# Performance work log

Measured on AMD Instinct MI355X. Metric: run time of the kernel, lower is better.

Reference implementation:

```python
import jax, jax.numpy as jnp
import numpy as np

N_NODES = 50000
TEMPERATURE = 1.0


def _gcn_norm(edge_index, n_nodes):
    src, dst = edge_index[0], edge_index[1]
    ones = jnp.ones(src.shape[0], dtype=jnp.float32)
    deg = 1.0 + jax.ops.segment_sum(ones, dst, num_segments=n_nodes)  # +1 for self loop
    dinv = jax.lax.rsqrt(deg)
    norm_e = dinv[src] * dinv[dst]          # symmetric edge norm
    self_norm = 1.0 / deg                   # self-loop contribution deg^-1
    return norm_e, self_norm


def _gcn_layer(x, W, b, src, dst, norm_e, self_norm, n_nodes):
    h = x @ W                                # [N, d_out]
    msg = h[src] * norm_e[:, None]           # gather + scale, [E, d_out]
    agg = jax.ops.segment_sum(msg, dst, num_segments=n_nodes)
    return agg + h * self_norm[:, None] + b


def setup_inputs() -> dict:
    key = jax.random.key(0)
    ks = jax.random.split(key, 8)
    n_feat, n_hid, n_layer, n_class = 128, 64, 4, 40
    n_edges = 800000
    x = jax.random.normal(ks[0], (N_NODES, n_feat), dtype=jnp.float32)
    edge_index = jax.random.randint(ks[1], (2, n_edges), 0, N_NODES, dtype=jnp.int64)
    s0 = 1.0 / np.sqrt(n_feat)
    s1 = 1.0 / np.sqrt(n_hid)
    W0 = jax.random.normal(ks[2], (n_feat, n_hid), dtype=jnp.float32) * s0
    b0 = jnp.zeros((n_hid,), dtype=jnp.float32)
    Ws = jax.random.normal(ks[3], (n_layer - 1, n_hid, n_hid), dtype=jnp.float32) * s1
    bs = jnp.zeros((n_layer - 1, n_hid), dtype=jnp.float32)
    Wout = jax.random.normal(ks[4], (n_hid, n_class), dtype=jnp.float32) * s1
    bout = jnp.zeros((n_class,), dtype=jnp.float32)
    return {"x": x, "W0": W0, "b0": b0, "Ws": Ws, "bs": bs,
            "Wout": Wout, "bout": bout, "edge_index": edge_index}


def reference(x, W0, b0, Ws, bs, Wout, bout, edge_index):
    src, dst = edge_index[0], edge_index[1]
    norm_e, self_norm = _gcn_norm(edge_index, N_NODES)

    x_ = jax.lax.stop_gradient(x)  # x.clone().detach()
    hs, hs_ = [], []
    n_layer = Ws.shape[0] + 1
    for l in range(n_layer):
        W = W0 if l == 0 else Ws[l - 1]
        b = b0 if l == 0 else bs[l - 1]
        h = _gcn_layer(x, W, b, src, dst, norm_e, self_norm, N_NODES)
        h_ = _gcn_layer(x_, W, b, src, dst, norm_e, self_norm, N_NODES)
        # vanilla skip: x <- h; ReLU; dropout disabled (eval mode)
        x = jax.nn.relu(h)
        x_ = jax.nn.relu(h_)
        hs.append(x)
        hs_.append(x_)

    H = jnp.stack(hs, axis=1)    # [N, L, d]
    H_ = jnp.stack(hs_, axis=1)  # [N, L, d]
    # local dot-product kernel attention over layers
    scores = jnp.sum(H * H_, axis=-1) / TEMPERATURE          # [N, L]
    alpha = jax.nn.softmax(scores, axis=-1)                   # [N, L]
    h = jnp.einsum("nl,nld->nd", alpha, H)                    # [N, d]
    return h @ Wout + bout                                     # [N, n_class]
```

## Files before the change

kernel.cpp:

```cpp
#include <hip/hip_runtime.h>
#include <hip/hip_fp16.h>

#define N_NODES 50000
#define N_HID   64
#define N_LAYER 4
#define N_CLASS 40
#define N_EDGES 800000

#define BSHIFT 8
#define BSIZE  256
#define NBUCK  ((N_NODES + BSIZE - 1) / BSIZE)
#define BPAD   16
#define EPT    16
#define BKCHUNK (256 * EPT)
#define NBBLK  ((N_EDGES + BKCHUNK - 1) / BKCHUNK)

#define SCAP  5120
#define PBK   (SCAP + 15 * BSIZE)
#define DUMMY N_NODES


__global__ void k_zerob(int* __restrict__ bcur, __half* __restrict__ hdA,
                        __half* __restrict__ hdB) {
    int t = threadIdx.x;
    if (t < NBUCK) bcur[t * BPAD] = t * SCAP;
    if (t < 64) {
        hdA[(size_t)N_NODES * 64 + t] = __float2half(0.f);
        hdB[(size_t)N_NODES * 64 + t] = __float2half(0.f);
    }
}


__global__ void k_bucket(const int* __restrict__ src, const int* __restrict__ dst,
                         int* __restrict__ bcur, unsigned int* __restrict__ stag) {
    __shared__ int lhist[NBUCK];
    __shared__ int gbase[NBUCK];
    int t = threadIdx.x;
    for (int i = t; i < NBUCK; i += 256) lhist[i] = 0;
    __syncthreads();

    int base = blockIdx.x * BKCHUNK;
    unsigned int rec[EPT];
    int br[EPT];
#pragma unroll
    for (int i = 0; i < EPT; i++) {
        int e = base + i * 256 + t;
        if (e < N_EDGES) {
            int d = dst[e], s = src[e];
            int b = d >> BSHIFT;
            int r = atomicAdd(&lhist[b], 1);
            rec[i] = ((unsigned int)d << 16) | (unsigned int)s;
            br[i]  = (b << 16) | r;
        } else {
            br[i] = -1;
        }
    }
    __syncthreads();
    for (int i = t; i < NBUCK; i += 256) {
        int c = lhist[i];
        gbase[i] = c ? atomicAdd(&bcur[i * BPAD], c) : 0;
    }
    __syncthreads();
#pragma unroll
    for (int i = 0; i < EPT; i++) {
        if (br[i] >= 0) {
            int b = br[i] >> 16, r = br[i] & 0xffff;
            stag[gbase[b] + r] = rec[i];
        }
    }
}


__global__ void k_csr2(const unsigned int* __restrict__ stag, const int* __restrict__ bcur,
                       int* __restrict__ cnt, int* __restrict__ pcurg,
                       float* __restrict__ dinv, unsigned short* __restrict__ csr16) {
    __shared__ int lcnt[BSIZE], ltmp[BSIZE], lcur[BSIZE];
    int b = blockIdx.x, t = threadIdx.x;
    int bstart = b * SCAP;
    int bend   = bcur[b * BPAD];
    lcnt[t] = 0;
    __syncthreads();
    for (int i = bstart + t; i < bend; i += 256)
        atomicAdd(&lcnt[(stag[i] >> 16) & (BSIZE - 1)], 1);
    __syncthreads();
    int v = lcnt[t];
    int p = (v + 15) & ~15;
    ltmp[t] = p;
    __syncthreads();
    for (int off = 1; off < 256; off <<= 1) {
        int u = (t >= off) ? ltmp[t - off] : 0;
        __syncthreads();
        ltmp[t] += u;
        __syncthreads();
    }
    int pstart = b * PBK + ltmp[t] - p;
    lcur[t] = pstart;
    int node = (b << BSHIFT) + t;
    if (node < N_NODES) {
        cnt[node]   = v;
        pcurg[node] = pstart;
        dinv[node]  = rsqrtf((float)(v + 1));
    }
    __syncthreads();
    for (int i = bstart + t; i < bend; i += 256) {
        unsigned int rec = stag[i];
        int pos = atomicAdd(&lcur[(rec >> 16) & (BSIZE - 1)], 1);
        csr16[pos] = (unsigned short)rec;
    }
    for (int i = v; i < p; i++)
        csr16[pstart + i] = (unsigned short)DUMMY;
}


__global__ __launch_bounds__(256) void k_gemm0(const float* __restrict__ A,
                                               const float* __restrict__ W,
                                               const float* __restrict__ dinv,
                                               __half* __restrict__ hd) {
    __shared__ float As[16][128];
    int tid = threadIdx.x;
    int j  = tid & 63;
    int nl = tid >> 6;
    int node0 = blockIdx.x * 16;

    const float4* srcp = (const float4*)(A + (size_t)node0 * 128);
    float4* dstp = (float4*)&As[0][0];
    for (int idx = tid; idx < 16 * 128 / 4; idx += 256) dstp[idx] = srcp[idx];
    __syncthreads();

    float acc[4] = {0.f, 0.f, 0.f, 0.f};
#pragma unroll
    for (int k = 0; k < 128; k += 4) {
        float4 a0 = *(const float4*)&As[nl * 4 + 0][k];
        float4 a1 = *(const float4*)&As[nl * 4 + 1][k];
        float4 a2 = *(const float4*)&As[nl * 4 + 2][k];
        float4 a3 = *(const float4*)&As[nl * 4 + 3][k];
        float w0 = W[(k + 0) * 64 + j];
        float w1 = W[(k + 1) * 64 + j];
        float w2 = W[(k + 2) * 64 + j];
        float w3 = W[(k + 3) * 64 + j];
        acc[0] = fmaf(a0.w, w3, fmaf(a0.z, w2, fmaf(a0.y, w1, fmaf(a0.x, w0, acc[0]))));
        acc[1] = fmaf(a1.w, w3, fmaf(a1.z, w2, fmaf(a1.y, w1, fmaf(a1.x, w0, acc[1]))));
        acc[2] = fmaf(a2.w, w3, fmaf(a2.z, w2, fmaf(a2.y, w1, fmaf(a2.x, w0, acc[2]))));
        acc[3] = fmaf(a3.w, w3, fmaf(a3.z, w2, fmaf(a3.y, w1, fmaf(a3.x, w0, acc[3]))));
    }
#pragma unroll
    for (int i = 0; i < 4; i++) {
        int n = node0 + nl * 4 + i;
        hd[(size_t)n * 64 + j] = __float2half(acc[i] * dinv[n]);
    }
}


__device__ __forceinline__ float4 agg_node16(const uint2* __restrict__ hd2,
                                             const int* __restrict__ cnt,
                                             const int* __restrict__ pcur,
                                             const unsigned short* __restrict__ csr16,
                                             int n, int f, int par) {
    int k = pcur[n] + par * 4;
    int iters = (cnt[n] + 15) >> 4;
    float s0 = 0.f, s1 = 0.f, s2 = 0.f, s3 = 0.f;
    for (int it = 0; it < iters; ++it, k += 16) {
        uint2 idx = *(const uint2*)(csr16 + k);
        int a0 = idx.x & 0xffff, a1 = idx.x >> 16;
        int a2 = idx.y & 0xffff, a3 = idx.y >> 16;
        uint2 r0 = hd2[(size_t)a0 * 16 + f];
        uint2 r1 = hd2[(size_t)a1 * 16 + f];
        uint2 r2 = hd2[(size_t)a2 * 16 + f];
        uint2 r3 = hd2[(size_t)a3 * 16 + f];
        float2 p0 = __half22float2(*(const __half2*)&r0.x), q0 = __half22float2(*(const __half2*)&r0.y);
        float2 p1 = __half22float2(*(const __half2*)&r1.x), q1 = __half22float2(*(const __half2*)&r1.y);
        float2 p2 = __half22float2(*(const __half2*)&r2.x), q2 = __half22float2(*(const __half2*)&r2.y);
        float2 p3 = __half22float2(*(const __half2*)&r3.x), q3 = __half22float2(*(const __half2*)&r3.y);
        s0 += (p0.x + p1.x) + (p2.x + p3.x);
        s1 += (p0.y + p1.y) + (p2.y + p3.y);
        s2 += (q0.x + q1.x) + (q2.x + q3.x);
        s3 += (q0.y + q1.y) + (q2.y + q3.y);
    }
    s0 += __shfl_xor(s0, 16, 64); s1 += __shfl_xor(s1, 16, 64);
    s2 += __shfl_xor(s2, 16, 64); s3 += __shfl_xor(s3, 16, 64);
    s0 += __shfl_xor(s0, 32, 64); s1 += __shfl_xor(s1, 32, 64);
    s2 += __shfl_xor(s2, 32, 64); s3 += __shfl_xor(s3, 32, 64);
    return make_float4(s0, s1, s2, s3);
}


__global__ __launch_bounds__(256) void k_fused(const uint2* __restrict__ hd2_in,
                                               const float* __restrict__ b,
                                               const float* __restrict__ dinv,
                                               const int* __restrict__ cnt,
                                               const int* __restrict__ pcur,
                                               const unsigned short* __restrict__ csr16,
                                               const float* __restrict__ W,
                                               __half* __restrict__ hs_out,
                                               __half* __restrict__ hd_out) {
    __shared__ float As[4][64];
    int tid = threadIdx.x;
    int w = tid >> 6, lane = tid & 63;
    int f = lane & 15, par = lane >> 4;
    int node0 = blockIdx.x * 4;
    int n = node0 + w;

    float4 s = agg_node16(hd2_in, cnt, pcur, csr16, n, f, par);
    if (par == 0) {
        float dv = dinv[n];
        uint2 sr = hd2_in[(size_t)n * 16 + f];
        float2 sp = __half22float2(*(const __half2*)&sr.x);
        float2 sq = __half22float2(*(const __half2*)&sr.y);
        float o0 = fmaxf(fmaf(s.x + sp.x, dv, b[f * 4 + 0]), 0.f);
        float o1 = fmaxf(fmaf(s.y + sp.y, dv, b[f * 4 + 1]), 0.f);
        float o2 = fmaxf(fmaf(s.z + sq.x, dv, b[f * 4 + 2]), 0.f);
        float o3 = fmaxf(fmaf(s.w + sq.y, dv, b[f * 4 + 3]), 0.f);
        *(float4*)&As[w][f * 4] = make_float4(o0, o1, o2, o3);
        __half2 h0 = __halves2half2(__float2half(o0), __float2half(o1));
        __half2 h1 = __halves2half2(__float2half(o2), __float2half(o3));
        uint2 pk;
        pk.x = *(const unsigned int*)&h0;
        pk.y = *(const unsigned int*)&h1;
        ((uint2*)hs_out)[(size_t)n * 16 + f] = pk;
    }
    __syncthreads();

    if (tid < 64) {
        float acc[4] = {0.f, 0.f, 0.f, 0.f};
#pragma unroll
        for (int k = 0; k < 64; k += 4) {
            float4 a0 = *(const float4*)&As[0][k];
            float4 a1 = *(const float4*)&As[1][k];
            float4 a2 = *(const float4*)&As[2][k];
            float4 a3 = *(const float4*)&As[3][k];
            float w0 = W[(k + 0) * 64 + tid];
            float w1 = W[(k + 1) * 64 + tid];
            float w2 = W[(k + 2) * 64 + tid];
            float w3 = W[(k + 3) * 64 + tid];
            acc[0] = fmaf(a0.w, w3, fmaf(a0.z, w2, fmaf(a0.y, w1, fmaf(a0.x, w0, acc[0]))));
            acc[1] = fmaf(a1.w, w3, fmaf(a1.z, w2, fmaf(a1.y, w1, fmaf(a1.x, w0, acc[1]))));
            acc[2] = fmaf(a2.w, w3, fmaf(a2.z, w2, fmaf(a2.y, w1, fmaf(a2.x, w0, acc[2]))));
            acc[3] = fmaf(a3.w, w3, fmaf(a3.z, w2, fmaf(a3.y, w1, fmaf(a3.x, w0, acc[3]))));
        }
#pragma unroll
        for (int i = 0; i < 4; i++) {
            int nn = node0 + i;
            hd_out[(size_t)nn * 64 + tid] = __float2half(acc[i] * dinv[nn]);
        }
    }
}


__global__ __launch_bounds__(256) void k_last(const uint2* __restrict__ hd2_in,
                                              const float* __restrict__ b,
                                              const float* __restrict__ dinv,
                                              const int* __restrict__ cnt,
                                              const int* __restrict__ pcur,
                                              const unsigned short* __restrict__ csr16,
                                              const __half* __restrict__ hs16,
                                              const float* __restrict__ Wout,
                                              const float* __restrict__ bout,
                                              float* __restrict__ out) {
    __shared__ float As[4][64];
    int tid = threadIdx.x;
    int w = tid >> 6, lane = tid & 63;
    int f = lane & 15, par = lane >> 4;
    int node0 = blockIdx.x * 4;
    int n = node0 + w;

    float4 s = agg_node16(hd2_in, cnt, pcur, csr16, n, f, par);
    if (par == 0) {
        float dv = dinv[n];
        uint2 sr = hd2_in[(size_t)n * 16 + f];
        float2 sp = __half22float2(*(const __half2*)&sr.x);
        float2 sq = __half22float2(*(const __half2*)&sr.y);
        float o0 = fmaxf(fmaf(s.x + sp.x, dv, b[f * 4 + 0]), 0.f);
        float o1 = fmaxf(fmaf(s.y + sp.y, dv, b[f * 4 + 1]), 0.f);
        float o2 = fmaxf(fmaf(s.z + sq.x, dv, b[f * 4 + 2]), 0.f);
        float o3 = fmaxf(fmaf(s.w + sq.y, dv, b[f * 4 + 3]), 0.f);
        *(float4*)&As[w][f * 4] = make_float4(o0, o1, o2, o3);
    }
    __builtin_amdgcn_wave_barrier();

    float v[N_LAYER], sc[N_LAYER];
#pragma unroll
    for (int l = 0; l < 3; l++) {
        float val = __half2float(hs16[((size_t)l * N_NODES + n) * 64 + lane]);
        v[l]  = val;
        sc[l] = val * val;
    }
    v[3]  = As[w][lane];
    sc[3] = v[3] * v[3];
#pragma unroll
    for (int off = 32; off > 0; off >>= 1) {
#pragma unroll
        for (int l = 0; l < N_LAYER; l++) sc[l] += __shfl_xor(sc[l], off, 64);
    }
    float m = fmaxf(fmaxf(sc[0], sc[1]), fmaxf(sc[2], sc[3]));
    float e[N_LAYER];
    float sum = 0.f;
#pragma unroll
    for (int l = 0; l < N_LAYER; l++) { e[l] = __expf(sc[l] - m); sum += e[l]; }
    float inv = 1.f / sum;
    float bl = 0.f;
#pragma unroll
    for (int l = 0; l < N_LAYER; l++) bl = fmaf(e[l] * inv, v[l], bl);
    As[w][lane] = bl;
    __syncthreads();

    if (tid < 64 && tid < N_CLASS) {
        float acc[4] = {bout[tid], bout[tid], bout[tid], bout[tid]};
#pragma unroll
        for (int k = 0; k < 64; k += 4) {
            float4 a0 = *(const float4*)&As[0][k];
            float4 a1 = *(const float4*)&As[1][k];
            float4 a2 = *(const float4*)&As[2][k];
            float4 a3 = *(const float4*)&As[3][k];
            float w0 = Wout[(k + 0) * N_CLASS + tid];
            float w1 = Wout[(k + 1) * N_CLASS + tid];
            float w2 = Wout[(k + 2) * N_CLASS + tid];
            float w3 = Wout[(k + 3) * N_CLASS + tid];
            acc[0] = fmaf(a0.w, w3, fmaf(a0.z, w2, fmaf(a0.y, w1, fmaf(a0.x, w0, acc[0]))));
            acc[1] = fmaf(a1.w, w3, fmaf(a1.z, w2, fmaf(a1.y, w1, fmaf(a1.x, w0, acc[1]))));
            acc[2] = fmaf(a2.w, w3, fmaf(a2.z, w2, fmaf(a2.y, w1, fmaf(a2.x, w0, acc[2]))));
            acc[3] = fmaf(a3.w, w3, fmaf(a3.z, w2, fmaf(a3.y, w1, fmaf(a3.x, w0, acc[3]))));
        }
#pragma unroll
        for (int i = 0; i < 4; i++)
            out[(size_t)(node0 + i) * N_CLASS + tid] = acc[i];
    }
}


extern "C" void kernel_launch(void* const* d_in, const int* in_sizes, int n_in,
                              void* d_out, int out_size, void* d_ws, size_t ws_size,
                              hipStream_t stream) {
    const float* x    = (const float*)d_in[0];
    const float* W0   = (const float*)d_in[1];
    const float* b0   = (const float*)d_in[2];
    const float* Ws   = (const float*)d_in[3];
    const float* bs   = (const float*)d_in[4];
    const float* Wout = (const float*)d_in[5];
    const float* bout = (const float*)d_in[6];
    const int*   ei   = (const int*)d_in[7];
    const int* src = ei;
    const int* dst = ei + N_EDGES;
    float* out = (float*)d_out;

    int*            cnt   = (int*)d_ws;
    int*            pcur  = cnt + N_NODES;
    int*            bcur  = pcur + N_NODES;
    float*          dinv  = (float*)(bcur + NBUCK * BPAD);
    unsigned short* csr16 = (unsigned short*)(dinv + N_NODES);
    __half*         hdA   = (__half*)(csr16 + (size_t)NBUCK * PBK);
    __half*         hdB   = hdA + (size_t)(N_NODES + 1) * 64;
    __half*         hs16  = hdB + (size_t)(N_NODES + 1) * 64;
    unsigned int*   stag  = (unsigned int*)hs16;

    k_zerob <<<1, 256, 0, stream>>>(bcur, hdA, hdB);
    k_bucket<<<NBBLK, 256, 0, stream>>>(src, dst, bcur, stag);
    k_csr2  <<<NBUCK, 256, 0, stream>>>(stag, bcur, cnt, pcur, dinv, csr16);

    k_gemm0<<<N_NODES / 16, 256, 0, stream>>>(x, W0, dinv, hdA);

    const int NB = N_NODES / 4;

    k_fused<<<NB, 256, 0, stream>>>((const uint2*)hdA, b0, dinv, cnt, pcur, csr16,
                                    Ws + 0 * 64 * 64, hs16 + (size_t)0 * N_NODES * 64, hdB);
    k_fused<<<NB, 256, 0, stream>>>((const uint2*)hdB, bs + 0 * 64, dinv, cnt, pcur, csr16,
                                    Ws + 1 * 64 * 64, hs16 + (size_t)1 * N_NODES * 64, hdA);
    k_fused<<<NB, 256, 0, stream>>>((const uint2*)hdA, bs + 1 * 64, dinv, cnt, pcur, csr16,
                                    Ws + 2 * 64 * 64, hs16 + (size_t)2 * N_NODES * 64, hdB);
    k_last <<<NB, 256, 0, stream>>>((const uint2*)hdB, bs + 2 * 64, dinv, cnt, pcur, csr16,
                                    hs16, Wout, bout, out);
}
```

Baseline: 188.2 us.

## Split feature table into half-width column slabs and unfuse aggregation from GEMM

Stores the per-layer scaled features as two 32-column fp16 slabs, so each gather pass reads a smaller table (about 3.2 MB) that can stay in cache during the random neighbour gathers. Aggregation becomes its own kernel, run twice per layer (once per slab). The dense 64x64 transform moves to a separate GEMM kernel, and attention plus the output projection move to a standalone kernel. In exchange the CSR index stream is read twice per layer, there are more kernel launches, and hs is written and read back through global memory between the stages.

```diff
diff --git a/kernel.cpp b/kernel.cpp
--- a/kernel.cpp
+++ b/kernel.cpp
@@ -20,13 +20,13 @@
 #define DUMMY N_NODES
 
 
-__global__ void k_zerob(int* __restrict__ bcur, __half* __restrict__ hdA,
-                        __half* __restrict__ hdB) {
+__global__ void k_zerob(int* __restrict__ bcur, __half* __restrict__ hdLo,
+                        __half* __restrict__ hdHi) {
     int t = threadIdx.x;
     if (t < NBUCK) bcur[t * BPAD] = t * SCAP;
-    if (t < 64) {
-        hdA[(size_t)N_NODES * 64 + t] = __float2half(0.f);
-        hdB[(size_t)N_NODES * 64 + t] = __float2half(0.f);
+    if (t < 32) {
+        hdLo[(size_t)N_NODES * 32 + t] = __float2half(0.f);
+        hdHi[(size_t)N_NODES * 32 + t] = __float2half(0.f);
     }
 }
 
@@ -115,7 +115,8 @@
 __global__ __launch_bounds__(256) void k_gemm0(const float* __restrict__ A,
                                                const float* __restrict__ W,
                                                const float* __restrict__ dinv,
-                                               __half* __restrict__ hd) {
+                                               __half* __restrict__ hdLo,
+                                               __half* __restrict__ hdHi) {
     __shared__ float As[16][128];
     int tid = threadIdx.x;
     int j  = tid & 63;
@@ -146,146 +147,126 @@
 #pragma unroll
     for (int i = 0; i < 4; i++) {
         int n = node0 + nl * 4 + i;
-        hd[(size_t)n * 64 + j] = __float2half(acc[i] * dinv[n]);
-    }
-}
-
-
-__device__ __forceinline__ float4 agg_node16(const uint2* __restrict__ hd2,
+        float v = acc[i] * dinv[n];
+        if (j < 32) hdLo[(size_t)n * 32 + j]      = __float2half(v);
+        else        hdHi[(size_t)n * 32 + j - 32] = __float2half(v);
+    }
+}
+
+
+__global__ __launch_bounds__(256) void k_agg(const uint2* __restrict__ tbl,
+                                             const float* __restrict__ b32,
+                                             const float* __restrict__ dinv,
                                              const int* __restrict__ cnt,
                                              const int* __restrict__ pcur,
                                              const unsigned short* __restrict__ csr16,
-                                             int n, int f, int par) {
-    int k = pcur[n] + par * 4;
+                                             uint2* __restrict__ hs_out) {
+    int tid = threadIdx.x;
+    int w = tid >> 6, lane = tid & 63;
+    int f = lane & 7;
+    int par = lane >> 3;
+    int n = blockIdx.x * 4 + w;
+
+    int k = pcur[n] + par * 2;
     int iters = (cnt[n] + 15) >> 4;
     float s0 = 0.f, s1 = 0.f, s2 = 0.f, s3 = 0.f;
     for (int it = 0; it < iters; ++it, k += 16) {
-        uint2 idx = *(const uint2*)(csr16 + k);
-        int a0 = idx.x & 0xffff, a1 = idx.x >> 16;
-        int a2 = idx.y & 0xffff, a3 = idx.y >> 16;
-        uint2 r0 = hd2[(size_t)a0 * 16 + f];
-        uint2 r1 = hd2[(size_t)a1 * 16 + f];
-        uint2 r2 = hd2[(size_t)a2 * 16 + f];
-        uint2 r3 = hd2[(size_t)a3 * 16 + f];
+        unsigned int idx = *(const unsigned int*)(csr16 + k);
+        int a0 = idx & 0xffff, a1 = idx >> 16;
+        uint2 r0 = tbl[(size_t)a0 * 8 + f];
+        uint2 r1 = tbl[(size_t)a1 * 8 + f];
         float2 p0 = __half22float2(*(const __half2*)&r0.x), q0 = __half22float2(*(const __half2*)&r0.y);
         float2 p1 = __half22float2(*(const __half2*)&r1.x), q1 = __half22float2(*(const __half2*)&r1.y);
-        float2 p2 = __half22float2(*(const __half2*)&r2.x), q2 = __half22float2(*(const __half2*)&r2.y);
-        float2 p3 = __half22float2(*(const __half2*)&r3.x), q3 = __half22float2(*(const __half2*)&r3.y);
-        s0 += (p0.x + p1.x) + (p2.x + p3.x);
-        s1 += (p0.y + p1.y) + (p2.y + p3.y);
-        s2 += (q0.x + q1.x) + (q2.x + q3.x);
-        s3 += (q0.y + q1.y) + (q2.y + q3.y);
-    }
+        s0 += p0.x + p1.x;
+        s1 += p0.y + p1.y;
+        s2 += q0.x + q1.x;
+        s3 += q0.y + q1.y;
+    }
+    s0 += __shfl_xor(s0, 8, 64);  s1 += __shfl_xor(s1, 8, 64);
+    s2 += __shfl_xor(s2, 8, 64);  s3 += __shfl_xor(s3, 8, 64);
     s0 += __shfl_xor(s0, 16, 64); s1 += __shfl_xor(s1, 16, 64);
     s2 += __shfl_xor(s2, 16, 64); s3 += __shfl_xor(s3, 16, 64);
     s0 += __shfl_xor(s0, 32, 64); s1 += __shfl_xor(s1, 32, 64);
     s2 += __shfl_xor(s2, 32, 64); s3 += __shfl_xor(s3, 32, 64);
-    return make_float4(s0, s1, s2, s3);
-}
-
-
-__global__ __launch_bounds__(256) void k_fused(const uint2* __restrict__ hd2_in,
-                                               const float* __restrict__ b,
-                                               const float* __restrict__ dinv,
-                                               const int* __restrict__ cnt,
-                                               const int* __restrict__ pcur,
-                                               const unsigned short* __restrict__ csr16,
-                                               const float* __restrict__ W,
-                                               __half* __restrict__ hs_out,
-                                               __half* __restrict__ hd_out) {
-    __shared__ float As[4][64];
-    int tid = threadIdx.x;
-    int w = tid >> 6, lane = tid & 63;
-    int f = lane & 15, par = lane >> 4;
-    int node0 = blockIdx.x * 4;
-    int n = node0 + w;
-
-    float4 s = agg_node16(hd2_in, cnt, pcur, csr16, n, f, par);
+
     if (par == 0) {
         float dv = dinv[n];
-        uint2 sr = hd2_in[(size_t)n * 16 + f];
+        uint2 sr = tbl[(size_t)n * 8 + f];
         float2 sp = __half22float2(*(const __half2*)&sr.x);
         float2 sq = __half22float2(*(const __half2*)&sr.y);
-        float o0 = fmaxf(fmaf(s.x + sp.x, dv, b[f * 4 + 0]), 0.f);
-        float o1 = fmaxf(fmaf(s.y + sp.y, dv, b[f * 4 + 1]), 0.f);
-        float o2 = fmaxf(fmaf(s.z + sq.x, dv, b[f * 4 + 2]), 0.f);
-        float o3 = fmaxf(fmaf(s.w + sq.y, dv, b[f * 4 + 3]), 0.f);
-        *(float4*)&As[w][f * 4] = make_float4(o0, o1, o2, o3);
+        float o0 = fmaxf(fmaf(s0 + sp.x, dv, b32[f * 4 + 0]), 0.f);
+        float o1 = fmaxf(fmaf(s1 + sp.y, dv, b32[f * 4 + 1]), 0.f);
+        float o2 = fmaxf(fmaf(s2 + sq.x, dv, b32[f * 4 + 2]), 0.f);
+        float o3 = fmaxf(fmaf(s3 + sq.y, dv, b32[f * 4 + 3]), 0.f);
         __half2 h0 = __halves2half2(__float2half(o0), __float2half(o1));
         __half2 h1 = __halves2half2(__float2half(o2), __float2half(o3));
         uint2 pk;
         pk.x = *(const unsigned int*)&h0;
         pk.y = *(const unsigned int*)&h1;
-        ((uint2*)hs_out)[(size_t)n * 16 + f] = pk;
-    }
-    __syncthreads();
-
-    if (tid < 64) {
-        float acc[4] = {0.f, 0.f, 0.f, 0.f};
-#pragma unroll
-        for (int k = 0; k < 64; k += 4) {
-            float4 a0 = *(const float4*)&As[0][k];
-            float4 a1 = *(const float4*)&As[1][k];
-            float4 a2 = *(const float4*)&As[2][k];
-            float4 a3 = *(const float4*)&As[3][k];
-            float w0 = W[(k + 0) * 64 + tid];
-            float w1 = W[(k + 1) * 64 + tid];
-            float w2 = W[(k + 2) * 64 + tid];
-            float w3 = W[(k + 3) * 64 + tid];
-            acc[0] = fmaf(a0.w, w3, fmaf(a0.z, w2, fmaf(a0.y, w1, fmaf(a0.x, w0, acc[0]))));
-            acc[1] = fmaf(a1.w, w3, fmaf(a1.z, w2, fmaf(a1.y, w1, fmaf(a1.x, w0, acc[1]))));
-            acc[2] = fmaf(a2.w, w3, fmaf(a2.z, w2, fmaf(a2.y, w1, fmaf(a2.x, w0, acc[2]))));
-            acc[3] = fmaf(a3.w, w3, fmaf(a3.z, w2, fmaf(a3.y, w1, fmaf(a3.x, w0, acc[3]))));
-        }
-#pragma unroll
-        for (int i = 0; i < 4; i++) {
-            int nn = node0 + i;
-            hd_out[(size_t)nn * 64 + tid] = __float2half(acc[i] * dinv[nn]);
-        }
-    }
-}
-
-
-__global__ __launch_bounds__(256) void k_last(const uint2* __restrict__ hd2_in,
-                                              const float* __restrict__ b,
+        hs_out[(size_t)n * 16 + f] = pk;
+    }
+}
+
+
+__global__ __launch_bounds__(256) void k_gemm(const uint2* __restrict__ hs,
+                                              const float* __restrict__ W,
                                               const float* __restrict__ dinv,
-                                              const int* __restrict__ cnt,
-                                              const int* __restrict__ pcur,
-                                              const unsigned short* __restrict__ csr16,
-                                              const __half* __restrict__ hs16,
+                                              __half* __restrict__ hdLo,
+                                              __half* __restrict__ hdHi) {
+    __shared__ float As[16][64];
+    int tid = threadIdx.x;
+    int node0 = blockIdx.x * 16;
+
+    uint2 h = hs[(size_t)node0 * 16 + tid];
+    float2 pa = __half22float2(*(const __half2*)&h.x);
+    float2 pb = __half22float2(*(const __half2*)&h.y);
+    *(float4*)&As[tid >> 4][(tid & 15) * 4] = make_float4(pa.x, pa.y, pb.x, pb.y);
+    __syncthreads();
+
+    int j  = tid & 63;
+    int nl = tid >> 6;
+    float acc[4] = {0.f, 0.f, 0.f, 0.f};
+#pragma unroll
+    for (int k = 0; k < 64; k += 4) {
+        float4 a0 = *(const float4*)&As[nl * 4 + 0][k];
+        float4 a1 = *(const float4*)&As[nl * 4 + 1][k];
+        float4 a2 = *(const float4*)&As[nl * 4 + 2][k];
+        float4 a3 = *(const float4*)&As[nl * 4 + 3][k];
+        float w0 = W[(k + 0) * 64 + j];
+        float w1 = W[(k + 1) * 64 + j];
+        float w2 = W[(k + 2) * 64 + j];
+        float w3 = W[(k + 3) * 64 + j];
+        acc[0] = fmaf(a0.w, w3, fmaf(a0.z, w2, fmaf(a0.y, w1, fmaf(a0.x, w0, acc[0]))));
+        acc[1] = fmaf(a1.w, w3, fmaf(a1.z, w2, fmaf(a1.y, w1, fmaf(a1.x, w0, acc[1]))));
+        acc[2] = fmaf(a2.w, w3, fmaf(a2.z, w2, fmaf(a2.y, w1, fmaf(a2.x, w0, acc[2]))));
+        acc[3] = fmaf(a3.w, w3, fmaf(a3.z, w2, fmaf(a3.y, w1, fmaf(a3.x, w0, acc[3]))));
+    }
+#pragma unroll
+    for (int i = 0; i < 4; i++) {
+        int n = node0 + nl * 4 + i;
+        float v = acc[i] * dinv[n];
+        if (j < 32) hdLo[(size_t)n * 32 + j]      = __float2half(v);
+        else        hdHi[(size_t)n * 32 + j - 32] = __float2half(v);
+    }
+}
+
+
+__global__ __launch_bounds__(256) void k_attn(const __half* __restrict__ hs16,
                                               const float* __restrict__ Wout,
                                               const float* __restrict__ bout,
                                               float* __restrict__ out) {
-    __shared__ float As[4][64];
-    int tid = threadIdx.x;
-    int w = tid >> 6, lane = tid & 63;
-    int f = lane & 15, par = lane >> 4;
-    int node0 = blockIdx.x * 4;
-    int n = node0 + w;
-
-    float4 s = agg_node16(hd2_in, cnt, pcur, csr16, n, f, par);
-    if (par == 0) {
-        float dv = dinv[n];
-        uint2 sr = hd2_in[(size_t)n * 16 + f];
-        float2 sp = __half22float2(*(const __half2*)&sr.x);
-        float2 sq = __half22float2(*(const __half2*)&sr.y);
-        float o0 = fmaxf(fmaf(s.x + sp.x, dv, b[f * 4 + 0]), 0.f);
-        float o1 = fmaxf(fmaf(s.y + sp.y, dv, b[f * 4 + 1]), 0.f);
-        float o2 = fmaxf(fmaf(s.z + sq.x, dv, b[f * 4 + 2]), 0.f);
-        float o3 = fmaxf(fmaf(s.w + sq.y, dv, b[f * 4 + 3]), 0.f);
-        *(float4*)&As[w][f * 4] = make_float4(o0, o1, o2, o3);
-    }
-    __builtin_amdgcn_wave_barrier();
+    __shared__ float blend[4][64];
+    int j  = threadIdx.x & 63;
+    int nl = threadIdx.x >> 6;
+    int n  = blockIdx.x * 4 + nl;
 
     float v[N_LAYER], sc[N_LAYER];
 #pragma unroll
-    for (int l = 0; l < 3; l++) {
-        float val = __half2float(hs16[((size_t)l * N_NODES + n) * 64 + lane]);
+    for (int l = 0; l < N_LAYER; l++) {
+        float val = __half2float(hs16[((size_t)l * N_NODES + n) * 64 + j]);
         v[l]  = val;
         sc[l] = val * val;
     }
-    v[3]  = As[w][lane];
-    sc[3] = v[3] * v[3];
 #pragma unroll
     for (int off = 32; off > 0; off >>= 1) {
 #pragma unroll
@@ -300,29 +281,15 @@
     float bl = 0.f;
 #pragma unroll
     for (int l = 0; l < N_LAYER; l++) bl = fmaf(e[l] * inv, v[l], bl);
-    As[w][lane] = bl;
-    __syncthreads();
-
-    if (tid < 64 && tid < N_CLASS) {
-        float acc[4] = {bout[tid], bout[tid], bout[tid], bout[tid]};
-#pragma unroll
-        for (int k = 0; k < 64; k += 4) {
-            float4 a0 = *(const float4*)&As[0][k];
-            float4 a1 = *(const float4*)&As[1][k];
-            float4 a2 = *(const float4*)&As[2][k];
-            float4 a3 = *(const float4*)&As[3][k];
-            float w0 = Wout[(k + 0) * N_CLASS + tid];
-            float w1 = Wout[(k + 1) * N_CLASS + tid];
-            float w2 = Wout[(k + 2) * N_CLASS + tid];
-            float w3 = Wout[(k + 3) * N_CLASS + tid];
-            acc[0] = fmaf(a0.w, w3, fmaf(a0.z, w2, fmaf(a0.y, w1, fmaf(a0.x, w0, acc[0]))));
-            acc[1] = fmaf(a1.w, w3, fmaf(a1.z, w2, fmaf(a1.y, w1, fmaf(a1.x, w0, acc[1]))));
-            acc[2] = fmaf(a2.w, w3, fmaf(a2.z, w2, fmaf(a2.y, w1, fmaf(a2.x, w0, acc[2]))));
-            acc[3] = fmaf(a3.w, w3, fmaf(a3.z, w2, fmaf(a3.y, w1, fmaf(a3.x, w0, acc[3]))));
-        }
-#pragma unroll
-        for (int i = 0; i < 4; i++)
-            out[(size_t)(node0 + i) * N_CLASS + tid] = acc[i];
+    blend[nl][j] = bl;
+    __syncthreads();
+
+    if (j < N_CLASS) {
+        float o = bout[j];
+#pragma unroll
+        for (int k = 0; k < 64; k++)
+            o = fmaf(blend[nl][k], Wout[k * N_CLASS + j], o);
+        out[(size_t)n * N_CLASS + j] = o;
     }
 }
 
@@ -347,25 +314,31 @@
     int*            bcur  = pcur + N_NODES;
     float*          dinv  = (float*)(bcur + NBUCK * BPAD);
     unsigned short* csr16 = (unsigned short*)(dinv + N_NODES);
-    __half*         hdA   = (__half*)(csr16 + (size_t)NBUCK * PBK);
-    __half*         hdB   = hdA + (size_t)(N_NODES + 1) * 64;
-    __half*         hs16  = hdB + (size_t)(N_NODES + 1) * 64;
+    __half*         hdLo  = (__half*)(csr16 + (size_t)NBUCK * PBK);
+    __half*         hdHi  = hdLo + (size_t)(N_NODES + 1) * 32;
+    __half*         hs16  = hdHi + (size_t)(N_NODES + 1) * 32;
     unsigned int*   stag  = (unsigned int*)hs16;
 
-    k_zerob <<<1, 256, 0, stream>>>(bcur, hdA, hdB);
+    k_zerob <<<1, 256, 0, stream>>>(bcur, hdLo, hdHi);
     k_bucket<<<NBBLK, 256, 0, stream>>>(src, dst, bcur, stag);
     k_csr2  <<<NBUCK, 256, 0, stream>>>(stag, bcur, cnt, pcur, dinv, csr16);
 
-    k_gemm0<<<N_NODES / 16, 256, 0, stream>>>(x, W0, dinv, hdA);
+    k_gemm0<<<N_NODES / 16, 256, 0, stream>>>(x, W0, dinv, hdLo, hdHi);
 
     const int NB = N_NODES / 4;
 
-    k_fused<<<NB, 256, 0, stream>>>((const uint2*)hdA, b0, dinv, cnt, pcur, csr16,
-                                    Ws + 0 * 64 * 64, hs16 + (size_t)0 * N_NODES * 64, hdB);
-    k_fused<<<NB, 256, 0, stream>>>((const uint2*)hdB, bs + 0 * 64, dinv, cnt, pcur, csr16,
-                                    Ws + 1 * 64 * 64, hs16 + (size_t)1 * N_NODES * 64, hdA);
-    k_fused<<<NB, 256, 0, stream>>>((const uint2*)hdA, bs + 1 * 64, dinv, cnt, pcur, csr16,
-                                    Ws + 2 * 64 * 64, hs16 + (size_t)2 * N_NODES * 64, hdB);
-    k_last <<<NB, 256, 0, stream>>>((const uint2*)hdB, bs + 2 * 64, dinv, cnt, pcur, csr16,
-                                    hs16, Wout, bout, out);
-}
+    for (int l = 0; l < N_LAYER; l++) {
+        const float* b = (l == 0) ? b0 : bs + (size_t)(l - 1) * 64;
+        __half* hs_l = hs16 + (size_t)l * N_NODES * 64;
+        k_agg<<<NB, 256, 0, stream>>>((const uint2*)hdLo, b, dinv, cnt, pcur, csr16,
+                                      (uint2*)hs_l + 0);
+        k_agg<<<NB, 256, 0, stream>>>((const uint2*)hdHi, b + 32, dinv, cnt, pcur, csr16,
+                                      (uint2*)hs_l + 8);
+        if (l < N_LAYER - 1)
+            k_gemm<<<N_NODES / 16, 256, 0, stream>>>((const uint2*)hs_l,
+                                                     Ws + (size_t)l * 64 * 64, dinv,
+                                                     hdLo, hdHi);
+    }
+
+    k_attn<<<NB, 256, 0, stream>>>(hs16, Wout, bout, out);
+}
```

Result: slower. 402.8 us (+114.0%).
